# Optimization experiments

Measured on AMD Instinct MI355X. Metric: run time of the kernel, lower is better.

Reference implementation:

```python
import jax, jax.numpy as jnp
import numpy as np

DIM = 1024
HEADS = 16
DIM_HEAD = 64
INNER = HEADS * DIM_HEAD  # 1024


def setup_inputs() -> dict:
    key = jax.random.key(0)
    ks = jax.random.split(key, 6)
    B, N = 4, 2048
    x = jax.random.normal(ks[0], (B, N, DIM), dtype=jnp.float32)
    ln_gamma = jnp.ones((DIM,), jnp.float32)
    ln_beta = jnp.zeros((DIM,), jnp.float32)
    # nn.Linear weights stored [out, in]; apply as x @ W.T
    w_qkv = jax.random.normal(ks[1], (3 * INNER, DIM), dtype=jnp.float32) * (1.0 / np.sqrt(DIM))
    w_out = jax.random.normal(ks[2], (DIM, INNER), dtype=jnp.float32) * (1.0 / np.sqrt(INNER))
    b_out = jax.random.normal(ks[3], (DIM,), dtype=jnp.float32) * 0.01
    return {"x": x, "ln_gamma": ln_gamma, "ln_beta": ln_beta,
            "w_qkv": w_qkv, "w_out": w_out, "b_out": b_out}


def reference(x, ln_gamma, ln_beta, w_qkv, w_out, b_out):
    B, N, _ = x.shape
    scale = DIM_HEAD ** -0.5
    # LayerNorm (eps=1e-5, matching torch default)
    mu = jnp.mean(x, axis=-1, keepdims=True)
    var = jnp.mean(jnp.square(x - mu), axis=-1, keepdims=True)
    xn = (x - mu) * jax.lax.rsqrt(var + 1e-5) * ln_gamma + ln_beta
    qkv = xn @ w_qkv.T  # [B, N, 3*INNER]
    q, k, v = jnp.split(qkv, 3, axis=-1)
    # [B, H, N, Dh]
    def heads(t):
        return t.reshape(B, N, HEADS, DIM_HEAD).transpose(0, 2, 1, 3)
    q, k, v = heads(q), heads(k), heads(v)
    attn = jnp.einsum('bhnd,bhmd->bhnm', q, k) * scale
    attn = jax.nn.softmax(attn, axis=-1)
    out = jnp.einsum('bhnm,bhmd->bhnd', attn, v)
    out = out.transpose(0, 2, 1, 3).reshape(B, N, INNER)
    return out @ w_out.T + b_out
```

## Files before the change

### kernel.cpp

```cpp
#include <hip/hip_runtime.h>

typedef unsigned short u16;
typedef unsigned int u32;
typedef __attribute__((ext_vector_type(8))) short bf16x8;
typedef __attribute__((ext_vector_type(4))) float f32x4;
typedef __attribute__((ext_vector_type(16))) float f32x16;
typedef __attribute__((ext_vector_type(4))) unsigned int u32x4;

#define DIM   1024
#define NSEQ  2048
#define BATCH 4
#define HEADS 16
#define DH    64

__device__ __forceinline__ u16 f2bf(float f) {
    unsigned int u = __builtin_bit_cast(unsigned int, f);
    u += 0x7fffu + ((u >> 16) & 1u);
    return (u16)(u >> 16);
}

__device__ __forceinline__ u32 pkbf(float lo, float hi) {
    u32 r;
    asm("s_nop 1\n\tv_cvt_pk_bf16_f32 %0, %1, %2" : "=v"(r) : "v"(lo), "v"(hi));
    return r;
}

__device__ __forceinline__ void pl32swap(u32& a, u32& b) {
    asm("v_permlane32_swap_b32 %0, %1" : "+v"(a), "+v"(b));
}

__device__ __forceinline__ void gload16(const void* g, void* l) {
    __builtin_amdgcn_global_load_lds((__attribute__((address_space(1))) unsigned int*)(g),
                                     (__attribute__((address_space(3))) unsigned int*)(l),
                                     16, 0, 0);
}

#define MFMA16(a, b, c) __builtin_amdgcn_mfma_f32_16x16x32_bf16(a, b, c, 0, 0, 0)
#define MFMA32(a, b, c) __builtin_amdgcn_mfma_f32_32x32x16_bf16(a, b, c, 0, 0, 0)

__global__ __launch_bounds__(256) void ln_kernel(const float* __restrict__ x,
                                                 const float* __restrict__ g,
                                                 const float* __restrict__ b,
                                                 u16* __restrict__ xn) {
    int row = blockIdx.x;
    int tid = threadIdx.x;
    const float4 v = ((const float4*)(x + (size_t)row * DIM))[tid];
    float s  = v.x + v.y + v.z + v.w;
    float s2 = v.x * v.x + v.y * v.y + v.z * v.z + v.w * v.w;
#pragma unroll
    for (int o = 32; o; o >>= 1) { s += __shfl_xor(s, o); s2 += __shfl_xor(s2, o); }
    __shared__ float red[8];
    int wid = tid >> 6, lane = tid & 63;
    if (lane == 0) { red[wid] = s; red[4 + wid] = s2; }
    __syncthreads();
    s  = red[0] + red[1] + red[2] + red[3];
    s2 = red[4] + red[5] + red[6] + red[7];
    float mu  = s * (1.0f / DIM);
    float var = s2 * (1.0f / DIM) - mu * mu;
    float rs  = rsqrtf(var + 1e-5f);
    float4 gv = ((const float4*)g)[tid];
    float4 bv = ((const float4*)b)[tid];
    ushort4 o4 = make_ushort4(f2bf((v.x - mu) * rs * gv.x + bv.x),
                              f2bf((v.y - mu) * rs * gv.y + bv.y),
                              f2bf((v.z - mu) * rs * gv.z + bv.z),
                              f2bf((v.w - mu) * rs * gv.w + bv.w));
    ((ushort4*)(xn + (size_t)row * DIM))[tid] = o4;
}

__global__ __launch_bounds__(256) void castw(const float* __restrict__ wqkv,
                                             const float* __restrict__ wout,
                                             u16* __restrict__ wq,
                                             u16* __restrict__ wo) {
    int i = blockIdx.x * 256 + threadIdx.x;
    int e = i * 4;
    if (e < 3 * DIM * DIM) {
        float4 v = *(const float4*)(wqkv + e);
        float sc = (e < DIM * DIM) ? (0.125f * 1.44269504f) : 1.0f;
        *(ushort4*)(wq + e) = make_ushort4(f2bf(v.x * sc), f2bf(v.y * sc),
                                           f2bf(v.z * sc), f2bf(v.w * sc));
    } else {
        int e2 = e - 3 * DIM * DIM;
        float4 v = *(const float4*)(wout + e2);
        *(ushort4*)(wo + e2) = make_ushort4(f2bf(v.x), f2bf(v.y), f2bf(v.z), f2bf(v.w));
    }
}

__global__ __launch_bounds__(256) void gemm_qkv(const u16* __restrict__ A,
                                                const u16* __restrict__ Bw,
                                                u16* __restrict__ qb,
                                                u16* __restrict__ kb,
                                                u16* __restrict__ vtb) {
    __shared__ __align__(16) u16 As[2][128 * 32];
    __shared__ __align__(16) u16 Bs[2][128 * 32];
    const int K = DIM;
    int m0 = blockIdx.x * 128, n0 = blockIdx.y * 128;
    int tid = threadIdx.x, lane = tid & 63, wid = tid >> 6;
    int wr = wid >> 1, wc = wid & 1;
    f32x4 acc[4][4] = {};

#define GSTAGE(bi, k0) do {                                                              \
        _Pragma("unroll")                                                                \
        for (int j = 0; j < 2; ++j) {                                                    \
            int e = j * 256 + tid;                                                       \
            int cs = (e & 3) ^ ((e >> 3) & 3);                    \
            gload16(A  + (size_t)(m0 + (e >> 2)) * K + (k0) + cs * 8,                    \
                    &As[bi][j * 2048 + wid * 512]);                                      \
            gload16(Bw + (size_t)(n0 + (e >> 2)) * K + (k0) + cs * 8,                    \
                    &Bs[bi][j * 2048 + wid * 512]);                                      \
        }                                                                                \
    } while (0)

    GSTAGE(0, 0);
    __syncthreads();
    for (int kt = 0; kt < 32; ++kt) {
        int cur = kt & 1;
        if (kt < 31) GSTAGE(1 - cur, (kt + 1) * 32);
        bf16x8 a[4], b[4];
#pragma unroll
        for (int mi = 0; mi < 4; ++mi) {
            int r = wr * 64 + mi * 16 + (lane & 15);
            a[mi] = *(const bf16x8*)&As[cur][r * 32 + (((lane >> 4) ^ ((r >> 1) & 3)) << 3)];
        }
#pragma unroll
        for (int ni = 0; ni < 4; ++ni) {
            int r = wc * 64 + ni * 16 + (lane & 15);
            b[ni] = *(const bf16x8*)&Bs[cur][r * 32 + (((lane >> 4) ^ ((r >> 1) & 3)) << 3)];
        }
#pragma unroll
        for (int mi = 0; mi < 4; ++mi)
#pragma unroll
            for (int ni = 0; ni < 4; ++ni)
                acc[mi][ni] = MFMA16(a[mi], b[ni], acc[mi][ni]);
        __syncthreads();
    }
#undef GSTAGE
#pragma unroll
    for (int mi = 0; mi < 4; ++mi)
#pragma unroll
        for (int ni = 0; ni < 4; ++ni)
#pragma unroll
            for (int r = 0; r < 4; ++r) {
                int m = m0 + wr * 64 + mi * 16 + (lane >> 4) * 4 + r;
                int n = n0 + wc * 64 + ni * 16 + (lane & 15);
                u16 val = f2bf(acc[mi][ni][r]);
                int part = n >> 10, w = n & 1023, h = w >> 6, d = w & 63;
                int bidx = m >> 11, pos = m & 2047, bh = bidx * HEADS + h;
                if (part == 0)      qb[((size_t)bh * NSEQ + pos) * DH + d] = val;
                else if (part == 1) kb[((size_t)bh * NSEQ + pos) * DH + d] = val;
                else                vtb[((size_t)bh * DH + d) * NSEQ + pos] = val;
            }
}

__global__ __launch_bounds__(512, 4) void attn_kernel(const u16* __restrict__ qb,
                                                      const u16* __restrict__ kb,
                                                      const u16* __restrict__ vtb,
                                                      u16* __restrict__ ob) {
    __shared__ __align__(16) u16 Ks[2][64 * 64];
    __shared__ __align__(16) u16 Vs[2][64 * 64];
    int bh = blockIdx.x, qt = blockIdx.y;
    int tid = threadIdx.x, lane = tid & 63, wid = tid >> 6;
    int l31 = lane & 31, hi = lane >> 5, key = l31 & 7;

    const size_t kbase = (size_t)bh * NSEQ * DH;
    const size_t vbase = (size_t)bh * DH * NSEQ;

    int sr  = tid >> 3;
    int sc8 = (tid & 7) ^ (sr & 7);

#define STAGE(bi, kv0) do {                                                            \
        gload16(kb  + kbase + (size_t)((kv0) + sr) * DH + sc8 * 8, &Ks[bi][wid * 512]); \
        gload16(vtb + vbase + (size_t)sr * NSEQ + (kv0) + sc8 * 8, &Vs[bi][wid * 512]); \
    } while (0)

    int qrow = qt * 256 + wid * 32 + l31;
    const u16* qp = qb + ((size_t)bh * NSEQ + qrow) * DH + 8 * hi;
    bf16x8 aq[4];
#pragma unroll
    for (int kd = 0; kd < 4; ++kd)
        aq[kd] = *(const bf16x8*)(qp + 16 * kd);

    const bf16x8 ones8 = {(short)0x3F80, (short)0x3F80, (short)0x3F80, (short)0x3F80,
                          (short)0x3F80, (short)0x3F80, (short)0x3F80, (short)0x3F80};

    f32x16 oacc[2] = {};
    f32x16 lacc = {};

    STAGE(0, 0);
    __syncthreads();

    for (int t = 0; t < 32; ++t) {
        int cur = t & 1;
        if (t < 31) STAGE(1 - cur, (t + 1) * 64);

        f32x16 s[2] = {};
#pragma unroll
        for (int kt = 0; kt < 2; ++kt)
#pragma unroll
            for (int kd = 0; kd < 4; ++kd) {
                bf16x8 bk = *(const bf16x8*)&Ks[cur][(kt * 32 + l31) * 64 + (((2 * kd + hi) ^ key) << 3)];
                s[kt] = MFMA32(bk, aq[kd], s[kt]);
            }

#pragma unroll
        for (int kt = 0; kt < 2; ++kt)
#pragma unroll
            for (int i = 0; i < 16; ++i)
                s[kt][i] = __builtin_amdgcn_exp2f(s[kt][i]);

#pragma unroll
        for (int kt = 0; kt < 2; ++kt) {
            u32 A0 = pkbf(s[kt][0],  s[kt][1]),  B0 = pkbf(s[kt][2],  s[kt][3]);
            u32 C0 = pkbf(s[kt][4],  s[kt][5]),  D0 = pkbf(s[kt][6],  s[kt][7]);
            pl32swap(A0, C0); pl32swap(B0, D0);
            u32x4 wv0 = {A0, B0, C0, D0};
            bf16x8 pf0 = __builtin_bit_cast(bf16x8, wv0);
            u32 A1 = pkbf(s[kt][8],  s[kt][9]),  B1 = pkbf(s[kt][10], s[kt][11]);
            u32 C1 = pkbf(s[kt][12], s[kt][13]), D1 = pkbf(s[kt][14], s[kt][15]);
            pl32swap(A1, C1); pl32swap(B1, D1);
            u32x4 wv1 = {A1, B1, C1, D1};
            bf16x8 pf1 = __builtin_bit_cast(bf16x8, wv1);
            lacc = MFMA32(ones8, pf0, lacc);
            lacc = MFMA32(ones8, pf1, lacc);
#pragma unroll
            for (int dt = 0; dt < 2; ++dt) {
                int rbase = (dt * 32 + l31) * 64;
                bf16x8 vb0 = *(const bf16x8*)&Vs[cur][rbase + (((4 * kt + hi) ^ key) << 3)];
                oacc[dt] = MFMA32(vb0, pf0, oacc[dt]);
                bf16x8 vb1 = *(const bf16x8*)&Vs[cur][rbase + (((4 * kt + 2 + hi) ^ key) << 3)];
                oacc[dt] = MFMA32(vb1, pf1, oacc[dt]);
            }
        }
        __syncthreads();
    }

    float inv = 1.0f / lacc[0];
    int bb = bh >> 4, h = bh & 15;
    u16* orow = ob + ((size_t)(bb * NSEQ + qrow)) * DIM + h * 64 + 4 * hi;
#pragma unroll
    for (int dt = 0; dt < 2; ++dt)
#pragma unroll
        for (int gg = 0; gg < 4; ++gg) {
            uint2 st;
            st.x = pkbf(oacc[dt][4 * gg] * inv,     oacc[dt][4 * gg + 1] * inv);
            st.y = pkbf(oacc[dt][4 * gg + 2] * inv, oacc[dt][4 * gg + 3] * inv);
            *(uint2*)(orow + dt * 32 + gg * 8) = st;
        }
#undef STAGE
}

__global__ __launch_bounds__(256) void gemm_out(const u16* __restrict__ A,
                                                const u16* __restrict__ Bw,
                                                const float* __restrict__ bias,
                                                float* __restrict__ out) {
    __shared__ __align__(16) u16 As[2][128 * 32];
    __shared__ __align__(16) u16 Bs[2][128 * 32];
    const int K = DIM;
    int m0 = blockIdx.x * 128, n0 = blockIdx.y * 128;
    int tid = threadIdx.x, lane = tid & 63, wid = tid >> 6;
    int wr = wid >> 1, wc = wid & 1;
    f32x4 acc[4][4] = {};

#define GSTAGE(bi, k0) do {                                                              \
        _Pragma("unroll")                                                                \
        for (int j = 0; j < 2; ++j) {                                                    \
            int e = j * 256 + tid;                                                       \
            int cs = (e & 3) ^ ((e >> 3) & 3);                                           \
            gload16(A  + (size_t)(m0 + (e >> 2)) * K + (k0) + cs * 8,                    \
                    &As[bi][j * 2048 + wid * 512]);                                      \
            gload16(Bw + (size_t)(n0 + (e >> 2)) * K + (k0) + cs * 8,                    \
                    &Bs[bi][j * 2048 + wid * 512]);                                      \
        }                                                                                \
    } while (0)

    GSTAGE(0, 0);
    __syncthreads();
    for (int kt = 0; kt < 32; ++kt) {
        int cur = kt & 1;
        if (kt < 31) GSTAGE(1 - cur, (kt + 1) * 32);
        bf16x8 a[4], b[4];
#pragma unroll
        for (int mi = 0; mi < 4; ++mi) {
            int r = wr * 64 + mi * 16 + (lane & 15);
            a[mi] = *(const bf16x8*)&As[cur][r * 32 + (((lane >> 4) ^ ((r >> 1) & 3)) << 3)];
        }
#pragma unroll
        for (int ni = 0; ni < 4; ++ni) {
            int r = wc * 64 + ni * 16 + (lane & 15);
            b[ni] = *(const bf16x8*)&Bs[cur][r * 32 + (((lane >> 4) ^ ((r >> 1) & 3)) << 3)];
        }
#pragma unroll
        for (int mi = 0; mi < 4; ++mi)
#pragma unroll
            for (int ni = 0; ni < 4; ++ni)
                acc[mi][ni] = MFMA16(a[mi], b[ni], acc[mi][ni]);
        __syncthreads();
    }
#undef GSTAGE
#pragma unroll
    for (int mi = 0; mi < 4; ++mi)
#pragma unroll
        for (int ni = 0; ni < 4; ++ni) {
            int n = n0 + wc * 64 + ni * 16 + (lane & 15);
            float bv = bias[n];
#pragma unroll
            for (int r = 0; r < 4; ++r) {
                int m = m0 + wr * 64 + mi * 16 + (lane >> 4) * 4 + r;
                out[(size_t)m * DIM + n] = acc[mi][ni][r] + bv;
            }
        }
}

extern "C" void kernel_launch(void* const* d_in, const int* in_sizes, int n_in,
                              void* d_out, int out_size, void* d_ws, size_t ws_size,
                              hipStream_t stream) {
    const float* x    = (const float*)d_in[0];
    const float* g    = (const float*)d_in[1];
    const float* be   = (const float*)d_in[2];
    const float* wqkv = (const float*)d_in[3];
    const float* wout = (const float*)d_in[4];
    const float* bout = (const float*)d_in[5];
    float* out = (float*)d_out;

    char* ws = (char*)d_ws;
    const size_t MB = 1024u * 1024u;
    u16* xn  = (u16*)(ws);
    u16* wq  = (u16*)(ws + 16 * MB);
    u16* wo  = (u16*)(ws + 22 * MB);
    u16* qb  = (u16*)(ws + 24 * MB);
    u16* kb  = (u16*)(ws + 40 * MB);
    u16* vtb = (u16*)(ws + 56 * MB);
    u16* ao  = xn;

    ln_kernel<<<8192, 256, 0, stream>>>(x, g, be, xn);
    castw<<<4096, 256, 0, stream>>>(wqkv, wout, wq, wo);
    gemm_qkv<<<dim3(64, 24), 256, 0, stream>>>(xn, wq, qb, kb, vtb);
    attn_kernel<<<dim3(64, 8), 512, 0, stream>>>(qb, kb, vtb, ao);
    gemm_out<<<dim3(64, 8), 256, 0, stream>>>(ao, wo, bout, out);
}
```

Before: 205.5 us.

## Deepen GEMM global-to-LDS pipeline to four buffers with vmcnt waits

Both the QKV and output projection GEMMs move from a double-buffered LDS pipeline to a four-buffer ring, keeping three K-tiles in flight. The full __syncthreads is replaced by explicit s_waitcnt vmcnt counts plus a bare s_barrier, so each step waits only for the oldest stage. The aim is to hide more global-load latency behind the MFMA work. In exchange, LDS per block doubles to 64 KB, which can lower occupancy, and correctness now depends on the hand-tuned vmcnt counts matching the number of loads each stage issues.

```diff
diff --git a/kernel.cpp b/kernel.cpp
--- a/kernel.cpp
+++ b/kernel.cpp
@@ -90,8 +90,8 @@
                                                 u16* __restrict__ qb,
                                                 u16* __restrict__ kb,
                                                 u16* __restrict__ vtb) {
-    __shared__ __align__(16) u16 As[2][128 * 32];
-    __shared__ __align__(16) u16 Bs[2][128 * 32];
+    __shared__ __align__(16) u16 As[4][128 * 32];
+    __shared__ __align__(16) u16 Bs[4][128 * 32];
     const int K = DIM;
     int m0 = blockIdx.x * 128, n0 = blockIdx.y * 128;
     int tid = threadIdx.x, lane = tid & 63, wid = tid >> 6;
@@ -111,10 +111,13 @@
     } while (0)
 
     GSTAGE(0, 0);
-    __syncthreads();
+    GSTAGE(1, 32);
+    GSTAGE(2, 64);
+    asm volatile("s_waitcnt vmcnt(8)" ::: "memory");
+    __builtin_amdgcn_s_barrier();
+
     for (int kt = 0; kt < 32; ++kt) {
-        int cur = kt & 1;
-        if (kt < 31) GSTAGE(1 - cur, (kt + 1) * 32);
+        int cur = kt & 3;
         bf16x8 a[4], b[4];
 #pragma unroll
         for (int mi = 0; mi < 4; ++mi) {
@@ -131,7 +134,16 @@
 #pragma unroll
             for (int ni = 0; ni < 4; ++ni)
                 acc[mi][ni] = MFMA16(a[mi], b[ni], acc[mi][ni]);
-        __syncthreads();
+
+        if (kt < 29) {
+            GSTAGE((kt + 3) & 3, (kt + 3) * 32);
+            asm volatile("s_waitcnt vmcnt(8)" ::: "memory");
+        } else if (kt == 29) {
+            asm volatile("s_waitcnt vmcnt(4)" ::: "memory");
+        } else {
+            asm volatile("s_waitcnt vmcnt(0)" ::: "memory");
+        }
+        __builtin_amdgcn_s_barrier();
     }
 #undef GSTAGE
 #pragma unroll
@@ -252,8 +264,8 @@
                                                 const u16* __restrict__ Bw,
                                                 const float* __restrict__ bias,
                                                 float* __restrict__ out) {
-    __shared__ __align__(16) u16 As[2][128 * 32];
-    __shared__ __align__(16) u16 Bs[2][128 * 32];
+    __shared__ __align__(16) u16 As[4][128 * 32];
+    __shared__ __align__(16) u16 Bs[4][128 * 32];
     const int K = DIM;
     int m0 = blockIdx.x * 128, n0 = blockIdx.y * 128;
     int tid = threadIdx.x, lane = tid & 63, wid = tid >> 6;
@@ -273,10 +285,13 @@
     } while (0)
 
     GSTAGE(0, 0);
-    __syncthreads();
+    GSTAGE(1, 32);
+    GSTAGE(2, 64);
+    asm volatile("s_waitcnt vmcnt(8)" ::: "memory");
+    __builtin_amdgcn_s_barrier();
+
     for (int kt = 0; kt < 32; ++kt) {
-        int cur = kt & 1;
-        if (kt < 31) GSTAGE(1 - cur, (kt + 1) * 32);
+        int cur = kt & 3;
         bf16x8 a[4], b[4];
 #pragma unroll
         for (int mi = 0; mi < 4; ++mi) {
@@ -293,7 +308,16 @@
 #pragma unroll
             for (int ni = 0; ni < 4; ++ni)
                 acc[mi][ni] = MFMA16(a[mi], b[ni], acc[mi][ni]);
-        __syncthreads();
+
+        if (kt < 29) {
+            GSTAGE((kt + 3) & 3, (kt + 3) * 32);
+            asm volatile("s_waitcnt vmcnt(8)" ::: "memory");
+        } else if (kt == 29) {
+            asm volatile("s_waitcnt vmcnt(4)" ::: "memory");
+        } else {
+            asm volatile("s_waitcnt vmcnt(0)" ::: "memory");
+        }
+        __builtin_amdgcn_s_barrier();
     }
 #undef GSTAGE
 #pragma unroll
```

Result: no change. 206.6 us (+0.6%).
